# Optimization experiments

Hardware: AMD Instinct MI355X
Metric: run time of the kernel (lower is better)

The kernel has to match this reference:

```python
import jax, jax.numpy as jnp
import numpy as np

NU, NI, D, NNZ = 80000, 40000, 128, 2000000
EPS = 1e-12


def _spmm(dst, src, vals, x, n):
    # sum_e vals[e] * x[src[e]] scattered to dst[e]; A is [n, x.shape[0]] in COO.
    return jax.ops.segment_sum(vals[:, None] * x[src], dst, num_segments=n)


def setup_inputs() -> dict:
    key = jax.random.key(0)
    ks = jax.random.split(key, 24)
    limit = float(np.sqrt(6.0 / (D + D)))  # xavier_uniform
    inp = {
        'user_embedding': jax.random.normal(ks[0], (NU, D), jnp.float32),
        'item_embedding': jax.random.normal(ks[1], (NI, D), jnp.float32),
        'uu_embed0': jax.random.normal(ks[2], (NU, D), jnp.float32),
        'ii_embed0': jax.random.normal(ks[3], (NI, D), jnp.float32),
        'uu_embed1': jax.random.normal(ks[4], (NU, D), jnp.float32),
        'ii_embed1': jax.random.normal(ks[5], (NI, D), jnp.float32),
        'uu_embed2': jax.random.normal(ks[6], (NU, D), jnp.float32),
        'ii_embed2': jax.random.normal(ks[7], (NI, D), jnp.float32),
        'u_w': jax.random.uniform(ks[8], (D, D), jnp.float32, -limit, limit),
        'i_w': jax.random.uniform(ks[9], (D, D), jnp.float32, -limit, limit),
    }
    for b in range(4):
        inp[f'rows{b}'] = jax.random.randint(ks[10 + 3 * b], (NNZ,), 0, NU, jnp.int32)
        inp[f'cols{b}'] = jax.random.randint(ks[11 + 3 * b], (NNZ,), 0, NI, jnp.int32)
        inp[f'vals{b}'] = jax.random.uniform(ks[12 + 3 * b], (NNZ,), jnp.float32)
    return inp


def reference(user_embedding, item_embedding, uu_embed0, ii_embed0, uu_embed1,
              ii_embed1, uu_embed2, ii_embed2, u_w, i_w,
              rows0, cols0, vals0, rows1, cols1, vals1,
              rows2, cols2, vals2, rows3, cols3, vals3):
    nu, ni = user_embedding.shape[0], item_embedding.shape[0]
    # behavior 0 = click, 1 = fav, 2 = cart, 3 = buy
    u0 = _spmm(rows0, cols0, vals0, ii_embed0, nu)
    i0 = _spmm(cols0, rows0, vals0, uu_embed0, ni)
    u1 = _spmm(rows1, cols1, vals1, ii_embed1, nu)
    i1 = _spmm(cols1, rows1, vals1, uu_embed1, ni)
    u2 = _spmm(rows2, cols2, vals2, ii_embed2, nu)
    i2 = _spmm(cols2, rows2, vals2, uu_embed2, ni)
    u3 = _spmm(rows3, cols3, vals3, item_embedding, nu)
    i3 = _spmm(cols3, rows3, vals3, user_embedding, ni)
    user_embeddings = jnp.stack([u0, u1, u2, u3], axis=0)  # [4, NU, D]
    item_embeddings = jnp.stack([i0, i1, i2, i3], axis=0)  # [4, NI, D]
    user_out = jax.nn.sigmoid(jnp.mean(user_embeddings, axis=0) @ u_w)
    item_out = jax.nn.sigmoid(jnp.mean(item_embeddings, axis=0) @ i_w)
    # F.normalize default: L2 over dim=1 (the node axis of the stacked tensor)
    def l2n(x):
        return x / jnp.maximum(jnp.linalg.norm(x, axis=1, keepdims=True), EPS)
    return (user_out, item_out, l2n(user_embeddings), l2n(item_embeddings),
            u0, i0, u1, i1, u2, i2)
```

## Files before the change

### kernel.cpp

```cpp
#include <hip/hip_runtime.h>

#define NU 80000
#define NI 40000
#define DD 128
#define NNZ_E 2000000
#define EPSN 1e-12f
#define BWROWS 256
#define NBU 313
#define NBI 157
#define NBPAD 320
#define BSTRIDE 336
#define BIN_E 8192
#define S2CAP 16384
#define NREP 4

struct EdgePtrs { const int* rows[4]; const int* cols[4]; const float* vals[4]; };

struct GM4 {
  const int* rp[4];
  const int2* pairs[4];
  const unsigned short* xt[4];
  float* out[4];
  float* dup[4];
  float* meanb;
  float* colsums;
  int cbase;
};

__device__ inline unsigned short f2bf(float f) {
  unsigned int u = __float_as_uint(f);
  u += 0x7FFFu + ((u >> 16) & 1u);
  return (unsigned short)(u >> 16);
}

__global__ __launch_bounds__(256) void conv_k(const float* __restrict__ src,
                                              unsigned short* __restrict__ dst, int n4) {
  int stride = blockDim.x * gridDim.x;
  for (int i = blockIdx.x * blockDim.x + threadIdx.x; i < n4; i += stride) {
    float4 f = ((const float4*)src)[i];
    ushort4 h;
    h.x = f2bf(f.x); h.y = f2bf(f.y); h.z = f2bf(f.z); h.w = f2bf(f.w);
    ((ushort4*)dst)[i] = h;
  }
}

__global__ __launch_bounds__(256) void histB_k(EdgePtrs ep, int* cntA) {
  int b = blockIdx.y;
  const int* __restrict__ rows = ep.rows[b];
  const int* __restrict__ cols = ep.cols[b];
  __shared__ int lh[NBU + NBI];
  for (int i = threadIdx.x; i < NBU + NBI; i += blockDim.x) lh[i] = 0;
  __syncthreads();
  int stride = blockDim.x * gridDim.x;
  for (int e = blockIdx.x * blockDim.x + threadIdx.x; e < NNZ_E; e += stride) {
    atomicAdd(&lh[rows[e] >> 8], 1);
    atomicAdd(&lh[NBU + (cols[e] >> 8)], 1);
  }
  __syncthreads();
  int* cu = cntA + (b * 2 + 0) * NBPAD;
  int* ci = cntA + (b * 2 + 1) * NBPAD;
  for (int i = threadIdx.x; i < NBU + NBI; i += blockDim.x) {
    int v = lh[i];
    if (v) {
      if (i < NBU) atomicAdd(&cu[i], v);
      else atomicAdd(&ci[i - NBU], v);
    }
  }
}

__global__ __launch_bounds__(512) void scanb_k(const int* cntA, int* baseA, int* gcurA) {
  __shared__ int wsums[9];
  int a = blockIdx.x;
  int dir = a & 1;
  int n = dir ? NBI : NBU;
  const int* cnt = cntA + a * NBPAD;
  int* base = baseA + a * BSTRIDE;
  int* gcur = gcurA + a * NBPAD;
  int t = threadIdx.x, lane = t & 63, w = t >> 6;
  int v = (t < n) ? cnt[t] : 0;
  int s = v;
  #pragma unroll
  for (int off = 1; off < 64; off <<= 1) {
    int x = __shfl_up(s, off);
    if (lane >= off) s += x;
  }
  if (lane == 63) wsums[w] = s;
  __syncthreads();
  if (t == 0) {
    int run = 0;
    for (int k = 0; k < 8; k++) { int x = wsums[k]; wsums[k] = run; run += x; }
    wsums[8] = run;
  }
  __syncthreads();
  int ex = wsums[w] + s - v;
  if (t < n) { base[t] = ex; gcur[t] = ex; }
  if (t == 0) base[n] = wsums[8];
}

__global__ __launch_bounds__(512) void bin_k(EdgePtrs ep, int b0, int* gcurA, int2* binned) {
  __shared__ int2 stage[BIN_E];
  __shared__ int lh[NBPAD], lscan[NBPAD], lcur[NBPAD], gpos[NBPAD];
  __shared__ int wsums[9];
  int dir = blockIdx.y, j = blockIdx.z, b = b0 + j;
  int NB = dir ? NBI : NBU;
  const int* __restrict__ dst = dir ? ep.cols[b] : ep.rows[b];
  const int* __restrict__ src = dir ? ep.rows[b] : ep.cols[b];
  const float* __restrict__ vals = ep.vals[b];
  int* gcur = gcurA + (b * 2 + dir) * NBPAD;
  int2* out = binned + ((size_t)j * 2 + dir) * NNZ_E;
  int t = threadIdx.x;
  int e0 = blockIdx.x * BIN_E;
  int nh = min(BIN_E, NNZ_E - e0);
  for (int i = t; i < NBPAD; i += 512) lh[i] = 0;
  __syncthreads();
  for (int i = t; i < nh; i += 512) atomicAdd(&lh[dst[e0 + i] >> 8], 1);
  __syncthreads();
  {
    int lane = t & 63, w = t >> 6;
    int v = (t < NB) ? lh[t] : 0;
    int s = v;
    #pragma unroll
    for (int off = 1; off < 64; off <<= 1) {
      int x = __shfl_up(s, off);
      if (lane >= off) s += x;
    }
    if (lane == 63) wsums[w] = s;
    __syncthreads();
    if (t == 0) {
      int run = 0;
      for (int k = 0; k < 8; k++) { int x = wsums[k]; wsums[k] = run; run += x; }
      wsums[8] = run;
    }
    __syncthreads();
    int ex = wsums[w] + s - v;
    if (t < NB) { lscan[t] = ex; lcur[t] = ex; gpos[t] = atomicAdd(&gcur[t], v); }
  }
  __syncthreads();
  for (int i = t; i < nh; i += 512) {
    int d = dst[e0 + i], s = src[e0 + i];
    int k = d >> 8;
    int pos = atomicAdd(&lcur[k], 1);
    stage[pos] = make_int2(s | ((d & 255) << 17), __float_as_int(vals[e0 + i]));
  }
  __syncthreads();
  int w = t >> 6, lane = t & 63;
  for (int k = w; k < NB; k += 8) {
    int c = lh[k];
    const int2* sp = stage + lscan[k];
    int2* gp = out + gpos[k];
    for (int i = lane; i < c; i += 64) gp[i] = sp[i];
  }
}

__global__ __launch_bounds__(512) void sort3_k(int* rpU, int* rpI, int b0,
                                               const int* baseA, int2* binned) {
  __shared__ int2 stage[S2CAP];
  __shared__ int lh[256];
  __shared__ int excl[257];
  __shared__ int lcur[256];
  __shared__ int wsums[5];
  int gb = blockIdx.x;
  int j = gb / (NBU + NBI);
  int r = gb - j * (NBU + NBI);
  int dir = (r >= NBU) ? 1 : 0;
  int k = dir ? (r - NBU) : r;
  int b = b0 + j;
  int n = dir ? NI : NU;
  int* rp = dir ? (rpI + (size_t)b * (NI + 1)) : (rpU + (size_t)b * (NU + 1));
  const int* base = baseA + (b * 2 + dir) * BSTRIDE;
  int2* bb = binned + ((size_t)j * 2 + dir) * NNZ_E;
  int row0 = k << 8;
  int nrows = min(BWROWS, n - row0);
  int base0 = base[k];
  int tot = base[k + 1] - base0;
  int t = threadIdx.x;
  if (t < 256) lh[t] = 0;
  __syncthreads();
  for (int i = t; i < tot; i += 512) atomicAdd(&lh[(bb[base0 + i].x >> 17) & 255], 1);
  __syncthreads();
  int v = 0, s = 0;
  if (t < 256) {
    int lane = t & 63, w = t >> 6;
    v = lh[t]; s = v;
    #pragma unroll
    for (int off = 1; off < 64; off <<= 1) {
      int x = __shfl_up(s, off);
      if (lane >= off) s += x;
    }
    if (lane == 63) wsums[w] = s;
  }
  __syncthreads();
  if (t == 0) {
    int run = 0;
    for (int q = 0; q < 4; q++) { int x = wsums[q]; wsums[q] = run; run += x; }
    wsums[4] = run;
  }
  __syncthreads();
  if (t < 256) {
    int ex = wsums[t >> 6] + s - v;
    excl[t] = ex; lcur[t] = ex;
  }
  if (t == 0) excl[256] = wsums[4];
  __syncthreads();
  if (t <= nrows) rp[row0 + t] = base0 + excl[t];
  for (int i = t; i < tot; i += 512) {
    int2 p = bb[base0 + i];
    int ld = (p.x >> 17) & 255;
    int pos = atomicAdd(&lcur[ld], 1);
    stage[pos] = make_int2(p.x & 0x1FFFF, p.y);
  }
  __syncthreads();
  for (int i = t; i < tot; i += 512) bb[base0 + i] = stage[i];
}

__global__ __launch_bounds__(256) void gather4_k(GM4 gm, int nrows, int ngroups) {
  int gid = blockIdx.x * 8 + (threadIdx.x >> 5);
  int lane = threadIdx.x & 31;
  int t = threadIdx.x;
  float4 sq0 = make_float4(0.f,0.f,0.f,0.f), sq1 = sq0, sq2 = sq0, sq3 = sq0;
  for (int r = gid; r < nrows; r += ngroups) {
    float4 mean = make_float4(0.f,0.f,0.f,0.f);
    #pragma unroll
    for (int b = 0; b < 4; b++) {
      const int* rp = gm.rp[b];
      const int2* __restrict__ pairs = gm.pairs[b];
      const ushort4* __restrict__ x4 = (const ushort4*)gm.xt[b];
      int beg = rp[r], end = rp[r + 1];
      float4 a0 = make_float4(0.f,0.f,0.f,0.f);
      float4 a1 = make_float4(0.f,0.f,0.f,0.f);
      int e = beg;
      for (; e + 3 < end; e += 4) {
        int2 p0 = pairs[e], p1 = pairs[e + 1], p2 = pairs[e + 2], p3 = pairs[e + 3];
        ushort4 h0 = x4[(size_t)p0.x * 32 + lane];
        ushort4 h1 = x4[(size_t)p1.x * 32 + lane];
        ushort4 h2 = x4[(size_t)p2.x * 32 + lane];
        ushort4 h3 = x4[(size_t)p3.x * 32 + lane];
        float v0 = __int_as_float(p0.y), v1 = __int_as_float(p1.y);
        float v2 = __int_as_float(p2.y), v3 = __int_as_float(p3.y);
        a0.x += v0 * __uint_as_float((unsigned)h0.x << 16);
        a0.y += v0 * __uint_as_float((unsigned)h0.y << 16);
        a0.z += v0 * __uint_as_float((unsigned)h0.z << 16);
        a0.w += v0 * __uint_as_float((unsigned)h0.w << 16);
        a1.x += v1 * __uint_as_float((unsigned)h1.x << 16);
        a1.y += v1 * __uint_as_float((unsigned)h1.y << 16);
        a1.z += v1 * __uint_as_float((unsigned)h1.z << 16);
        a1.w += v1 * __uint_as_float((unsigned)h1.w << 16);
        a0.x += v2 * __uint_as_float((unsigned)h2.x << 16);
        a0.y += v2 * __uint_as_float((unsigned)h2.y << 16);
        a0.z += v2 * __uint_as_float((unsigned)h2.z << 16);
        a0.w += v2 * __uint_as_float((unsigned)h2.w << 16);
        a1.x += v3 * __uint_as_float((unsigned)h3.x << 16);
        a1.y += v3 * __uint_as_float((unsigned)h3.y << 16);
        a1.z += v3 * __uint_as_float((unsigned)h3.z << 16);
        a1.w += v3 * __uint_as_float((unsigned)h3.w << 16);
      }
      for (; e < end; e++) {
        int2 p = pairs[e];
        ushort4 h = x4[(size_t)p.x * 32 + lane];
        float v = __int_as_float(p.y);
        a0.x += v * __uint_as_float((unsigned)h.x << 16);
        a0.y += v * __uint_as_float((unsigned)h.y << 16);
        a0.z += v * __uint_as_float((unsigned)h.z << 16);
        a0.w += v * __uint_as_float((unsigned)h.w << 16);
      }
      float4 res = make_float4(a0.x + a1.x, a0.y + a1.y, a0.z + a1.z, a0.w + a1.w);
      ((float4*)gm.out[b])[(size_t)r * 32 + lane] = res;
      if (gm.dup[b]) ((float4*)gm.dup[b])[(size_t)r * 32 + lane] = res;
      mean.x += res.x; mean.y += res.y; mean.z += res.z; mean.w += res.w;
      float4* sqp = (b == 0) ? &sq0 : (b == 1) ? &sq1 : (b == 2) ? &sq2 : &sq3;
      sqp->x += res.x * res.x; sqp->y += res.y * res.y;
      sqp->z += res.z * res.z; sqp->w += res.w * res.w;
    }
    mean.x *= 0.25f; mean.y *= 0.25f; mean.z *= 0.25f; mean.w *= 0.25f;
    ((float4*)gm.meanb)[(size_t)r * 32 + lane] = mean;
  }
  __shared__ float csq[512];
  csq[t] = 0.f; csq[t + 256] = 0.f;
  __syncthreads();
  int cb = lane * 4;
  atomicAdd(&csq[0 * 128 + cb + 0], sq0.x); atomicAdd(&csq[0 * 128 + cb + 1], sq0.y);
  atomicAdd(&csq[0 * 128 + cb + 2], sq0.z); atomicAdd(&csq[0 * 128 + cb + 3], sq0.w);
  atomicAdd(&csq[1 * 128 + cb + 0], sq1.x); atomicAdd(&csq[1 * 128 + cb + 1], sq1.y);
  atomicAdd(&csq[1 * 128 + cb + 2], sq1.z); atomicAdd(&csq[1 * 128 + cb + 3], sq1.w);
  atomicAdd(&csq[2 * 128 + cb + 0], sq2.x); atomicAdd(&csq[2 * 128 + cb + 1], sq2.y);
  atomicAdd(&csq[2 * 128 + cb + 2], sq2.z); atomicAdd(&csq[2 * 128 + cb + 3], sq2.w);
  atomicAdd(&csq[3 * 128 + cb + 0], sq3.x); atomicAdd(&csq[3 * 128 + cb + 1], sq3.y);
  atomicAdd(&csq[3 * 128 + cb + 2], sq3.z); atomicAdd(&csq[3 * 128 + cb + 3], sq3.w);
  __syncthreads();
  float* dst = gm.colsums + (blockIdx.x & (NREP - 1)) * 1024 + gm.cbase;
  atomicAdd(&dst[t], csq[t]);
  atomicAdd(&dst[t + 256], csq[t + 256]);
}

__global__ __launch_bounds__(256) void gather_k(const int* __restrict__ rp, const int2* __restrict__ pairs,
                                                const void* __restrict__ xt, int isbf,
                                                float* __restrict__ out1, float* __restrict__ out2,
                                                int nrows) {
  int gid = blockIdx.x * 8 + (threadIdx.x >> 5);
  int lane = threadIdx.x & 31;
  int tot = gridDim.x * 8;
  for (int r = gid; r < nrows; r += tot) {
    int beg = rp[r], end = rp[r + 1];
    float4 a0 = make_float4(0.f, 0.f, 0.f, 0.f);
    int e = beg;
    if (isbf) {
      const ushort4* __restrict__ x4 = (const ushort4*)xt;
      for (; e < end; e++) {
        int2 p = pairs[e];
        ushort4 h = x4[(size_t)p.x * 32 + lane];
        float v = __int_as_float(p.y);
        a0.x += v * __uint_as_float((unsigned)h.x << 16);
        a0.y += v * __uint_as_float((unsigned)h.y << 16);
        a0.z += v * __uint_as_float((unsigned)h.z << 16);
        a0.w += v * __uint_as_float((unsigned)h.w << 16);
      }
    } else {
      const float4* __restrict__ x4 = (const float4*)xt;
      for (; e < end; e++) {
        int2 p = pairs[e];
        float4 xv = x4[(size_t)p.x * 32 + lane];
        float v = __int_as_float(p.y);
        a0.x += v * xv.x; a0.y += v * xv.y; a0.z += v * xv.z; a0.w += v * xv.w;
      }
    }
    ((float4*)out1)[(size_t)r * 32 + lane] = a0;
    if (out2) ((float4*)out2)[(size_t)r * 32 + lane] = a0;
  }
}

__global__ __launch_bounds__(256) void gemm_sig_m(const float* __restrict__ mean,
                                                  const float* __restrict__ W, float* __restrict__ out,
                                                  int n) {
  __shared__ float wl[DD * DD];
  __shared__ float rl[8][DD];
  for (int i = threadIdx.x; i < DD * DD / 4; i += blockDim.x)
    ((float4*)wl)[i] = ((const float4*)W)[i];
  int c = threadIdx.x & 127;
  int g = threadIdx.x >> 7;
  int row0 = blockIdx.x * 64;
  for (int rr = 0; rr < 64; rr += 8) {
    int rbase = row0 + rr;
    __syncthreads();
    for (int i = threadIdx.x; i < 8 * DD; i += blockDim.x) {
      int lr = i >> 7, lc = i & 127;
      int r = rbase + lr;
      rl[lr][lc] = (r < n) ? mean[(size_t)r * DD + lc] : 0.f;
    }
    __syncthreads();
    float acc0 = 0.f, acc1 = 0.f, acc2 = 0.f, acc3 = 0.f;
    #pragma unroll 4
    for (int k = 0; k < DD; k++) {
      float wv = wl[k * DD + c];
      acc0 += rl[g * 4 + 0][k] * wv;
      acc1 += rl[g * 4 + 1][k] * wv;
      acc2 += rl[g * 4 + 2][k] * wv;
      acc3 += rl[g * 4 + 3][k] * wv;
    }
    float accs[4] = {acc0, acc1, acc2, acc3};
    for (int jj = 0; jj < 4; jj++) {
      int r = rbase + g * 4 + jj;
      if (r < n) out[(size_t)r * DD + c] = 1.f / (1.f + __expf(-accs[jj]));
    }
  }
}

__global__ __launch_bounds__(256) void gemm_sig_k(const float* __restrict__ x, size_t sstride,
                                                  const float* __restrict__ W, float* __restrict__ out,
                                                  int n) {
  __shared__ float wl[DD * DD];
  __shared__ float rl[8][DD];
  for (int i = threadIdx.x; i < DD * DD / 4; i += blockDim.x)
    ((float4*)wl)[i] = ((const float4*)W)[i];
  int c = threadIdx.x & 127;
  int g = threadIdx.x >> 7;
  int row0 = blockIdx.x * 64;
  for (int rr = 0; rr < 64; rr += 8) {
    int rbase = row0 + rr;
    __syncthreads();
    for (int i = threadIdx.x; i < 8 * DD; i += blockDim.x) {
      int lr = i >> 7, lc = i & 127;
      int r = rbase + lr;
      float m = 0.f;
      if (r < n) {
        size_t off = (size_t)r * DD + lc;
        m = 0.25f * (x[off] + x[off + sstride] + x[off + 2 * sstride] + x[off + 3 * sstride]);
      }
      rl[lr][lc] = m;
    }
    __syncthreads();
    float acc0 = 0.f, acc1 = 0.f, acc2 = 0.f, acc3 = 0.f;
    #pragma unroll 4
    for (int k = 0; k < DD; k++) {
      float wv = wl[k * DD + c];
      acc0 += rl[g * 4 + 0][k] * wv;
      acc1 += rl[g * 4 + 1][k] * wv;
      acc2 += rl[g * 4 + 2][k] * wv;
      acc3 += rl[g * 4 + 3][k] * wv;
    }
    float accs[4] = {acc0, acc1, acc2, acc3};
    for (int jj = 0; jj < 4; jj++) {
      int r = rbase + g * 4 + jj;
      if (r < n) out[(size_t)r * DD + c] = 1.f / (1.f + __expf(-accs[jj]));
    }
  }
}

__global__ __launch_bounds__(256) void colsq_k(const float* __restrict__ base, size_t sstride, int n,
                                               float* __restrict__ sums) {
  int b = blockIdx.y;
  const float* x = base + (size_t)b * sstride;
  int c = threadIdx.x & 127;
  int rh = threadIdx.x >> 7;
  float acc = 0.f;
  for (int r = blockIdx.x * 2 + rh; r < n; r += gridDim.x * 2) {
    float v = x[(size_t)r * DD + c];
    acc += v * v;
  }
  __shared__ float red[256];
  red[threadIdx.x] = acc;
  __syncthreads();
  if (threadIdx.x < 128) atomicAdd(&sums[b * DD + threadIdx.x], red[threadIdx.x] + red[threadIdx.x + 128]);
}

__global__ void inv_k(const float* __restrict__ sums, float* __restrict__ inv, int n, int nrep) {
  int i = blockIdx.x * blockDim.x + threadIdx.x;
  if (i < n) {
    float s = 0.f;
    for (int r = 0; r < nrep; r++) s += sums[r * 1024 + i];
    inv[i] = 1.f / fmaxf(sqrtf(s), EPSN);
  }
}

__global__ __launch_bounds__(256) void scaleall_k(float* __restrict__ l2nU, float* __restrict__ l2nI,
                                                  const float* __restrict__ invs) {
  int y = blockIdx.y;
  float4* b4;
  size_t slice;
  if (y < 4) { b4 = (float4*)l2nU + (size_t)y * NU * 32; slice = (size_t)NU * 32; }
  else { b4 = (float4*)l2nI + (size_t)(y - 4) * NI * 32; slice = (size_t)NI * 32; }
  const float4* inv4 = (const float4*)invs + (size_t)y * 32;
  size_t stride = (size_t)blockDim.x * gridDim.x;
  for (size_t i = (size_t)blockIdx.x * blockDim.x + threadIdx.x; i < slice; i += stride) {
    float4 s = inv4[i & 31];
    float4 v = b4[i];
    v.x *= s.x; v.y *= s.y; v.z *= s.z; v.w *= s.w;
    b4[i] = v;
  }
}

extern "C" void kernel_launch(void* const* d_in, const int* in_sizes, int n_in,
                              void* d_out, int out_size, void* d_ws, size_t ws_size,
                              hipStream_t stream) {
  const float* user_emb = (const float*)d_in[0];
  const float* item_emb = (const float*)d_in[1];
  const float* uu[4] = {(const float*)d_in[2], (const float*)d_in[4], (const float*)d_in[6], user_emb};
  const float* ii[4] = {(const float*)d_in[3], (const float*)d_in[5], (const float*)d_in[7], item_emb};
  const float* u_w = (const float*)d_in[8];
  const float* i_w = (const float*)d_in[9];
  EdgePtrs ep;
  for (int b = 0; b < 4; b++) {
    ep.rows[b] = (const int*)d_in[10 + 3 * b];
    ep.cols[b] = (const int*)d_in[11 + 3 * b];
    ep.vals[b] = (const float*)d_in[12 + 3 * b];
  }

  float* out = (float*)d_out;
  float* user_out = out;
  float* item_out = out + (size_t)NU * DD;
  float* l2nU = item_out + (size_t)NI * DD;
  float* l2nI = l2nU + (size_t)4 * NU * DD;
  float* u_slot[3];
  float* i_slot[3];
  {
    float* p = l2nI + (size_t)4 * NI * DD;
    for (int b = 0; b < 3; b++) {
      u_slot[b] = p; p += (size_t)NU * DD;
      i_slot[b] = p; p += (size_t)NI * DD;
    }
  }

  const size_t binsl = (size_t)2 * NNZ_E * 8;
  const size_t item_bf_sz = (size_t)4 * NI * DD * 2;
  const size_t user_bf_sz = (size_t)4 * NU * DD * 2;
  const size_t mean_sz = (size_t)(NU + NI) * DD * 4;
  const size_t smalls = 8u << 20;

  int batchB; bool bfI, bfU;
  if (ws_size >= 4 * binsl + item_bf_sz + user_bf_sz + mean_sz + smalls) { batchB = 4; bfI = bfU = true; }
  else if (ws_size >= 2 * binsl + item_bf_sz + user_bf_sz + smalls) { batchB = 2; bfI = bfU = true; }
  else if (ws_size >= binsl + item_bf_sz + user_bf_sz + smalls) { batchB = 1; bfI = bfU = true; }
  else if (ws_size >= binsl + item_bf_sz + smalls) { batchB = 1; bfI = true; bfU = false; }
  else { batchB = 1; bfI = bfU = false; }

  char* w = (char*)d_ws;
  auto alloc = [&](size_t bytes) {
    char* r = w;
    w += (bytes + 255) & ~(size_t)255;
    return r;
  };
  int2* binned = (int2*)alloc((size_t)batchB * binsl);
  unsigned short* itemB = bfI ? (unsigned short*)alloc(item_bf_sz) : nullptr;
  unsigned short* userB = bfU ? (unsigned short*)alloc(user_bf_sz) : nullptr;
  float* meanU = nullptr;
  float* meanI = nullptr;
  if (batchB == 4) {
    meanU = (float*)alloc((size_t)NU * DD * 4);
    meanI = (float*)alloc((size_t)NI * DD * 4);
  }
  int* cntA = (int*)alloc(4 * 2 * NBPAD * 4);
  int* baseA = (int*)alloc(4 * 2 * BSTRIDE * 4);
  int* gcurA = (int*)alloc(4 * 2 * NBPAD * 4);
  int* rpU = (int*)alloc((size_t)4 * (NU + 1) * 4);
  int* rpI = (int*)alloc((size_t)4 * (NI + 1) * 4);
  float* colsums = (float*)alloc(NREP * 1024 * 4);
  float* invs = (float*)alloc(8 * DD * 4);

  hipMemsetAsync(cntA, 0, 4 * 2 * NBPAD * 4, stream);
  histB_k<<<dim3(256, 4), 256, 0, stream>>>(ep, cntA);
  scanb_k<<<8, 512, 0, stream>>>(cntA, baseA, gcurA);

  const int nchunks = (NNZ_E + BIN_E - 1) / BIN_E;

  if (batchB == 4) {
    bin_k<<<dim3(nchunks, 2, 4), 512, 0, stream>>>(ep, 0, gcurA, binned);
    sort3_k<<<4 * (NBU + NBI), 512, 0, stream>>>(rpU, rpI, 0, baseA, binned);
    for (int b = 0; b < 4; b++)
      conv_k<<<512, 256, 0, stream>>>(ii[b], itemB + (size_t)b * NI * DD, NI * DD / 4);
    for (int b = 0; b < 4; b++)
      conv_k<<<512, 256, 0, stream>>>(uu[b], userB + (size_t)b * NU * DD, NU * DD / 4);
    hipMemsetAsync(colsums, 0, NREP * 1024 * 4, stream);

    GM4 gmU, gmI;
    for (int b = 0; b < 4; b++) {
      gmU.rp[b] = rpU + (size_t)b * (NU + 1);
      gmU.pairs[b] = binned + ((size_t)b * 2 + 0) * NNZ_E;
      gmU.xt[b] = itemB + (size_t)b * NI * DD;
      gmU.out[b] = l2nU + (size_t)b * NU * DD;
      gmU.dup[b] = (b < 3) ? u_slot[b] : nullptr;
      gmI.rp[b] = rpI + (size_t)b * (NI + 1);
      gmI.pairs[b] = binned + ((size_t)b * 2 + 1) * NNZ_E;
      gmI.xt[b] = userB + (size_t)b * NU * DD;
      gmI.out[b] = l2nI + (size_t)b * NI * DD;
      gmI.dup[b] = (b < 3) ? i_slot[b] : nullptr;
    }
    gmU.meanb = meanU; gmU.colsums = colsums; gmU.cbase = 0;
    gmI.meanb = meanI; gmI.colsums = colsums; gmI.cbase = 4 * DD;
    gather4_k<<<2500, 256, 0, stream>>>(gmU, NU, 2500 * 8);
    gather4_k<<<1250, 256, 0, stream>>>(gmI, NI, 1250 * 8);

    inv_k<<<4, 256, 0, stream>>>(colsums, invs, 8 * DD, NREP);
    gemm_sig_m<<<NU / 64, 256, 0, stream>>>(meanU, u_w, user_out, NU);
    gemm_sig_m<<<NI / 64, 256, 0, stream>>>(meanI, i_w, item_out, NI);
    scaleall_k<<<dim3(1024, 8), 256, 0, stream>>>(l2nU, l2nI, invs);
  } else {
    if (bfI)
      for (int b = 0; b < 4; b++)
        conv_k<<<512, 256, 0, stream>>>(ii[b], itemB + (size_t)b * NI * DD, NI * DD / 4);
    if (bfU)
      for (int b = 0; b < 4; b++)
        conv_k<<<512, 256, 0, stream>>>(uu[b], userB + (size_t)b * NU * DD, NU * DD / 4);
    for (int b0 = 0; b0 < 4; b0 += batchB) {
      bin_k<<<dim3(nchunks, 2, batchB), 512, 0, stream>>>(ep, b0, gcurA, binned);
      sort3_k<<<batchB * (NBU + NBI), 512, 0, stream>>>(rpU, rpI, b0, baseA, binned);
      for (int j = 0; j < batchB; j++) {
        int b = b0 + j;
        const void* xt0 = bfI ? (const void*)(itemB + (size_t)b * NI * DD) : (const void*)ii[b];
        const void* xt1 = bfU ? (const void*)(userB + (size_t)b * NU * DD) : (const void*)uu[b];
        gather_k<<<10000, 256, 0, stream>>>(rpU + (size_t)b * (NU + 1),
                                            binned + ((size_t)j * 2 + 0) * NNZ_E, xt0, bfI ? 1 : 0,
                                            l2nU + (size_t)b * NU * DD, (b < 3) ? u_slot[b] : nullptr, NU);
        gather_k<<<5000, 256, 0, stream>>>(rpI + (size_t)b * (NI + 1),
                                           binned + ((size_t)j * 2 + 1) * NNZ_E, xt1, bfU ? 1 : 0,
                                           l2nI + (size_t)b * NI * DD, (b < 3) ? i_slot[b] : nullptr, NI);
      }
    }
    gemm_sig_k<<<NU / 64, 256, 0, stream>>>(l2nU, (size_t)NU * DD, u_w, user_out, NU);
    gemm_sig_k<<<NI / 64, 256, 0, stream>>>(l2nI, (size_t)NI * DD, i_w, item_out, NI);
    hipMemsetAsync(colsums, 0, NREP * 1024 * 4, stream);
    colsq_k<<<dim3(512, 4), 256, 0, stream>>>(l2nU, (size_t)NU * DD, NU, colsums);
    colsq_k<<<dim3(512, 4), 256, 0, stream>>>(l2nI, (size_t)NI * DD, NI, colsums + 4 * DD);
    inv_k<<<4, 256, 0, stream>>>(colsums, invs, 8 * DD, 1);
    scaleall_k<<<dim3(1024, 8), 256, 0, stream>>>(l2nU, l2nI, invs);
  }
}
```

Measured before the change: 1.417 ms.

## Merge conversion, gather, GEMM and scale launches into fewer fused kernels

Replaces the eight per-behavior bf16 conversion launches with one 2D-grid launch. Merges the user and item gather kernels into one grid with direction chosen per block, each warp handling four fixed rows and loading behavior pointers once. Merges the two sigmoid GEMMs into one launch and folds the inverse-norm computation into the scaling kernel. This cuts launch count and lets user and item work share the GPU at once, at the cost of hardcoded grid sizes that assume NU and NI divide evenly into four-row warp groups.

```diff
diff --git a/kernel.cpp b/kernel.cpp
--- a/kernel.cpp
+++ b/kernel.cpp
@@ -13,24 +13,44 @@
 #define BIN_E 8192
 #define S2CAP 16384
 #define NREP 4
+#define GF_NBU 2500
+#define GF_NBI 1250
 
 struct EdgePtrs { const int* rows[4]; const int* cols[4]; const float* vals[4]; };
 
-struct GM4 {
-  const int* rp[4];
-  const int2* pairs[4];
-  const unsigned short* xt[4];
-  float* out[4];
-  float* dup[4];
-  float* meanb;
+struct GAll {
+  const int* rp[2][4];
+  const int2* pairs[2][4];
+  const unsigned short* xt[2][4];
+  float* out[2][4];
+  float* dup[2][4];
+  float* meanb[2];
   float* colsums;
-  int cbase;
 };
+
+struct ConvPtrs { const float* src[8]; unsigned short* dst[8]; int n4[8]; };
 
 __device__ inline unsigned short f2bf(float f) {
   unsigned int u = __float_as_uint(f);
   u += 0x7FFFu + ((u >> 16) & 1u);
   return (unsigned short)(u >> 16);
+}
+__device__ inline float bf2f(unsigned short h) {
+  return __uint_as_float((unsigned)h << 16);
+}
+
+__global__ __launch_bounds__(256) void convA_k(ConvPtrs cp) {
+  int y = blockIdx.y;
+  const float4* __restrict__ src = (const float4*)cp.src[y];
+  ushort4* __restrict__ dst = (ushort4*)cp.dst[y];
+  int n4 = cp.n4[y];
+  int stride = blockDim.x * gridDim.x;
+  for (int i = blockIdx.x * blockDim.x + threadIdx.x; i < n4; i += stride) {
+    float4 f = src[i];
+    ushort4 h;
+    h.x = f2bf(f.x); h.y = f2bf(f.y); h.z = f2bf(f.z); h.w = f2bf(f.w);
+    dst[i] = h;
+  }
 }
 
 __global__ __launch_bounds__(256) void conv_k(const float* __restrict__ src,
@@ -213,21 +233,31 @@
   for (int i = t; i < tot; i += 512) bb[base0 + i] = stage[i];
 }
 
-__global__ __launch_bounds__(256) void gather4_k(GM4 gm, int nrows, int ngroups) {
-  int gid = blockIdx.x * 8 + (threadIdx.x >> 5);
+__global__ __launch_bounds__(256) void gatherF_k(GAll g) {
+  int blk = blockIdx.x;
+  int dir = (blk >= GF_NBU) ? 1 : 0;
+  int lblk = dir ? (blk - GF_NBU) : blk;
+  int gid = lblk * 8 + (threadIdx.x >> 5);
   int lane = threadIdx.x & 31;
   int t = threadIdx.x;
-  float4 sq0 = make_float4(0.f,0.f,0.f,0.f), sq1 = sq0, sq2 = sq0, sq3 = sq0;
-  for (int r = gid; r < nrows; r += ngroups) {
-    float4 mean = make_float4(0.f,0.f,0.f,0.f);
+  int r0 = gid * 4;
+
+  float4 z = make_float4(0.f, 0.f, 0.f, 0.f);
+  float4 mean[4] = {z, z, z, z};
+  float4 sq[4] = {z, z, z, z};
+
+  #pragma unroll
+  for (int b = 0; b < 4; b++) {
+    const int* __restrict__ rp = g.rp[dir][b];
+    const int2* __restrict__ pairs = g.pairs[dir][b];
+    const ushort4* __restrict__ x4 = (const ushort4*)g.xt[dir][b];
+    float4* __restrict__ outp = (float4*)g.out[dir][b];
+    float4* __restrict__ dupp = (float4*)g.dup[dir][b];
     #pragma unroll
-    for (int b = 0; b < 4; b++) {
-      const int* rp = gm.rp[b];
-      const int2* __restrict__ pairs = gm.pairs[b];
-      const ushort4* __restrict__ x4 = (const ushort4*)gm.xt[b];
+    for (int k = 0; k < 4; k++) {
+      int r = r0 + k;
       int beg = rp[r], end = rp[r + 1];
-      float4 a0 = make_float4(0.f,0.f,0.f,0.f);
-      float4 a1 = make_float4(0.f,0.f,0.f,0.f);
+      float4 a0 = z, a1 = z;
       int e = beg;
       for (; e + 3 < end; e += 4) {
         int2 p0 = pairs[e], p1 = pairs[e + 1], p2 = pairs[e + 2], p3 = pairs[e + 3];
@@ -237,57 +267,50 @@
         ushort4 h3 = x4[(size_t)p3.x * 32 + lane];
         float v0 = __int_as_float(p0.y), v1 = __int_as_float(p1.y);
         float v2 = __int_as_float(p2.y), v3 = __int_as_float(p3.y);
-        a0.x += v0 * __uint_as_float((unsigned)h0.x << 16);
-        a0.y += v0 * __uint_as_float((unsigned)h0.y << 16);
-        a0.z += v0 * __uint_as_float((unsigned)h0.z << 16);
-        a0.w += v0 * __uint_as_float((unsigned)h0.w << 16);
-        a1.x += v1 * __uint_as_float((unsigned)h1.x << 16);
-        a1.y += v1 * __uint_as_float((unsigned)h1.y << 16);
-        a1.z += v1 * __uint_as_float((unsigned)h1.z << 16);
-        a1.w += v1 * __uint_as_float((unsigned)h1.w << 16);
-        a0.x += v2 * __uint_as_float((unsigned)h2.x << 16);
-        a0.y += v2 * __uint_as_float((unsigned)h2.y << 16);
-        a0.z += v2 * __uint_as_float((unsigned)h2.z << 16);
-        a0.w += v2 * __uint_as_float((unsigned)h2.w << 16);
-        a1.x += v3 * __uint_as_float((unsigned)h3.x << 16);
-        a1.y += v3 * __uint_as_float((unsigned)h3.y << 16);
-        a1.z += v3 * __uint_as_float((unsigned)h3.z << 16);
-        a1.w += v3 * __uint_as_float((unsigned)h3.w << 16);
+        a0.x += v0 * bf2f(h0.x); a0.y += v0 * bf2f(h0.y);
+        a0.z += v0 * bf2f(h0.z); a0.w += v0 * bf2f(h0.w);
+        a1.x += v1 * bf2f(h1.x); a1.y += v1 * bf2f(h1.y);
+        a1.z += v1 * bf2f(h1.z); a1.w += v1 * bf2f(h1.w);
+        a0.x += v2 * bf2f(h2.x); a0.y += v2 * bf2f(h2.y);
+        a0.z += v2 * bf2f(h2.z); a0.w += v2 * bf2f(h2.w);
+        a1.x += v3 * bf2f(h3.x); a1.y += v3 * bf2f(h3.y);
+        a1.z += v3 * bf2f(h3.z); a1.w += v3 * bf2f(h3.w);
       }
       for (; e < end; e++) {
         int2 p = pairs[e];
         ushort4 h = x4[(size_t)p.x * 32 + lane];
         float v = __int_as_float(p.y);
-        a0.x += v * __uint_as_float((unsigned)h.x << 16);
-        a0.y += v * __uint_as_float((unsigned)h.y << 16);
-        a0.z += v * __uint_as_float((unsigned)h.z << 16);
-        a0.w += v * __uint_as_float((unsigned)h.w << 16);
+        a0.x += v * bf2f(h.x); a0.y += v * bf2f(h.y);
+        a0.z += v * bf2f(h.z); a0.w += v * bf2f(h.w);
       }
       float4 res = make_float4(a0.x + a1.x, a0.y + a1.y, a0.z + a1.z, a0.w + a1.w);
-      ((float4*)gm.out[b])[(size_t)r * 32 + lane] = res;
-      if (gm.dup[b]) ((float4*)gm.dup[b])[(size_t)r * 32 + lane] = res;
-      mean.x += res.x; mean.y += res.y; mean.z += res.z; mean.w += res.w;
-      float4* sqp = (b == 0) ? &sq0 : (b == 1) ? &sq1 : (b == 2) ? &sq2 : &sq3;
-      sqp->x += res.x * res.x; sqp->y += res.y * res.y;
-      sqp->z += res.z * res.z; sqp->w += res.w * res.w;
-    }
-    mean.x *= 0.25f; mean.y *= 0.25f; mean.z *= 0.25f; mean.w *= 0.25f;
-    ((float4*)gm.meanb)[(size_t)r * 32 + lane] = mean;
+      outp[(size_t)r * 32 + lane] = res;
+      if (dupp) dupp[(size_t)r * 32 + lane] = res;
+      mean[k].x += res.x; mean[k].y += res.y; mean[k].z += res.z; mean[k].w += res.w;
+      sq[b].x += res.x * res.x; sq[b].y += res.y * res.y;
+      sq[b].z += res.z * res.z; sq[b].w += res.w * res.w;
+    }
+  }
+  float4* mb = (float4*)g.meanb[dir];
+  #pragma unroll
+  for (int k = 0; k < 4; k++) {
+    float4 m = mean[k];
+    m.x *= 0.25f; m.y *= 0.25f; m.z *= 0.25f; m.w *= 0.25f;
+    mb[(size_t)(r0 + k) * 32 + lane] = m;
   }
   __shared__ float csq[512];
   csq[t] = 0.f; csq[t + 256] = 0.f;
   __syncthreads();
   int cb = lane * 4;
-  atomicAdd(&csq[0 * 128 + cb + 0], sq0.x); atomicAdd(&csq[0 * 128 + cb + 1], sq0.y);
-  atomicAdd(&csq[0 * 128 + cb + 2], sq0.z); atomicAdd(&csq[0 * 128 + cb + 3], sq0.w);
-  atomicAdd(&csq[1 * 128 + cb + 0], sq1.x); atomicAdd(&csq[1 * 128 + cb + 1], sq1.y);
-  atomicAdd(&csq[1 * 128 + cb + 2], sq1.z); atomicAdd(&csq[1 * 128 + cb + 3], sq1.w);
-  atomicAdd(&csq[2 * 128 + cb + 0], sq2.x); atomicAdd(&csq[2 * 128 + cb + 1], sq2.y);
-  atomicAdd(&csq[2 * 128 + cb + 2], sq2.z); atomicAdd(&csq[2 * 128 + cb + 3], sq2.w);
-  atomicAdd(&csq[3 * 128 + cb + 0], sq3.x); atomicAdd(&csq[3 * 128 + cb + 1], sq3.y);
-  atomicAdd(&csq[3 * 128 + cb + 2], sq3.z); atomicAdd(&csq[3 * 128 + cb + 3], sq3.w);
-  __syncthreads();
-  float* dst = gm.colsums + (blockIdx.x & (NREP - 1)) * 1024 + gm.cbase;
+  #pragma unroll
+  for (int b = 0; b < 4; b++) {
+    atomicAdd(&csq[b * 128 + cb + 0], sq[b].x);
+    atomicAdd(&csq[b * 128 + cb + 1], sq[b].y);
+    atomicAdd(&csq[b * 128 + cb + 2], sq[b].z);
+    atomicAdd(&csq[b * 128 + cb + 3], sq[b].w);
+  }
+  __syncthreads();
+  float* dst = g.colsums + (blockIdx.x & (NREP - 1)) * 1024 + dir * 512;
   atomicAdd(&dst[t], csq[t]);
   atomicAdd(&dst[t + 256], csq[t + 256]);
 }
@@ -309,10 +332,8 @@
         int2 p = pairs[e];
         ushort4 h = x4[(size_t)p.x * 32 + lane];
         float v = __int_as_float(p.y);
-        a0.x += v * __uint_as_float((unsigned)h.x << 16);
-        a0.y += v * __uint_as_float((unsigned)h.y << 16);
-        a0.z += v * __uint_as_float((unsigned)h.z << 16);
-        a0.w += v * __uint_as_float((unsigned)h.w << 16);
+        a0.x += v * bf2f(h.x); a0.y += v * bf2f(h.y);
+        a0.z += v * bf2f(h.z); a0.w += v * bf2f(h.w);
       }
     } else {
       const float4* __restrict__ x4 = (const float4*)xt;
@@ -328,16 +349,22 @@
   }
 }
 
-__global__ __launch_bounds__(256) void gemm_sig_m(const float* __restrict__ mean,
-                                                  const float* __restrict__ W, float* __restrict__ out,
-                                                  int n) {
+__global__ __launch_bounds__(256) void gemm2_k(const float* __restrict__ meanU,
+                                               const float* __restrict__ meanI,
+                                               const float* __restrict__ u_w,
+                                               const float* __restrict__ i_w,
+                                               float* __restrict__ user_out,
+                                               float* __restrict__ item_out) {
   __shared__ float wl[DD * DD];
   __shared__ float rl[8][DD];
+  int blk = blockIdx.x;
+  const float* mean; const float* W; float* outp; int n; int row0;
+  if (blk < NU / 64) { mean = meanU; W = u_w; outp = user_out; n = NU; row0 = blk * 64; }
+  else { mean = meanI; W = i_w; outp = item_out; n = NI; row0 = (blk - NU / 64) * 64; }
   for (int i = threadIdx.x; i < DD * DD / 4; i += blockDim.x)
     ((float4*)wl)[i] = ((const float4*)W)[i];
   int c = threadIdx.x & 127;
   int g = threadIdx.x >> 7;
-  int row0 = blockIdx.x * 64;
   for (int rr = 0; rr < 64; rr += 8) {
     int rbase = row0 + rr;
     __syncthreads();
@@ -359,7 +386,7 @@
     float accs[4] = {acc0, acc1, acc2, acc3};
     for (int jj = 0; jj < 4; jj++) {
       int r = rbase + g * 4 + jj;
-      if (r < n) out[(size_t)r * DD + c] = 1.f / (1.f + __expf(-accs[jj]));
+      if (r < n) outp[(size_t)r * DD + c] = 1.f / (1.f + __expf(-accs[jj]));
     }
   }
 }
@@ -431,6 +458,32 @@
   }
 }
 
+__global__ __launch_bounds__(256) void scaleall2_k(float* __restrict__ l2nU, float* __restrict__ l2nI,
+                                                   const float* __restrict__ colsums) {
+  __shared__ float sinv[DD];
+  int y = blockIdx.y;
+  int t = threadIdx.x;
+  if (t < DD) {
+    float s = 0.f;
+    #pragma unroll
+    for (int rr = 0; rr < NREP; rr++) s += colsums[rr * 1024 + y * DD + t];
+    sinv[t] = 1.f / fmaxf(sqrtf(s), EPSN);
+  }
+  __syncthreads();
+  float4* b4;
+  size_t slice;
+  if (y < 4) { b4 = (float4*)l2nU + (size_t)y * NU * 32; slice = (size_t)NU * 32; }
+  else { b4 = (float4*)l2nI + (size_t)(y - 4) * NI * 32; slice = (size_t)NI * 32; }
+  const float4* inv4 = (const float4*)sinv;
+  size_t stride = (size_t)blockDim.x * gridDim.x;
+  for (size_t i = (size_t)blockIdx.x * blockDim.x + threadIdx.x; i < slice; i += stride) {
+    float4 s = inv4[i & 31];
+    float4 v = b4[i];
+    v.x *= s.x; v.y *= s.y; v.z *= s.z; v.w *= s.w;
+    b4[i] = v;
+  }
+}
+
 __global__ __launch_bounds__(256) void scaleall_k(float* __restrict__ l2nU, float* __restrict__ l2nI,
                                                   const float* __restrict__ invs) {
   int y = blockIdx.y;
@@ -524,34 +577,34 @@
   if (batchB == 4) {
     bin_k<<<dim3(nchunks, 2, 4), 512, 0, stream>>>(ep, 0, gcurA, binned);
     sort3_k<<<4 * (NBU + NBI), 512, 0, stream>>>(rpU, rpI, 0, baseA, binned);
-    for (int b = 0; b < 4; b++)
-      conv_k<<<512, 256, 0, stream>>>(ii[b], itemB + (size_t)b * NI * DD, NI * DD / 4);
-    for (int b = 0; b < 4; b++)
-      conv_k<<<512, 256, 0, stream>>>(uu[b], userB + (size_t)b * NU * DD, NU * DD / 4);
+
+    ConvPtrs cp;
+    for (int b = 0; b < 4; b++) {
+      cp.src[b] = ii[b]; cp.dst[b] = itemB + (size_t)b * NI * DD; cp.n4[b] = NI * DD / 4;
+      cp.src[4 + b] = uu[b]; cp.dst[4 + b] = userB + (size_t)b * NU * DD; cp.n4[4 + b] = NU * DD / 4;
+    }
+    convA_k<<<dim3(512, 8), 256, 0, stream>>>(cp);
     hipMemsetAsync(colsums, 0, NREP * 1024 * 4, stream);
 
-    GM4 gmU, gmI;
+    GAll g;
     for (int b = 0; b < 4; b++) {
-      gmU.rp[b] = rpU + (size_t)b * (NU + 1);
-      gmU.pairs[b] = binned + ((size_t)b * 2 + 0) * NNZ_E;
-      gmU.xt[b] = itemB + (size_t)b * NI * DD;
-      gmU.out[b] = l2nU + (size_t)b * NU * DD;
-      gmU.dup[b] = (b < 3) ? u_slot[b] : nullptr;
-      gmI.rp[b] = rpI + (size_t)b * (NI + 1);
-      gmI.pairs[b] = binned + ((size_t)b * 2 + 1) * NNZ_E;
-      gmI.xt[b] = userB + (size_t)b * NU * DD;
-      gmI.out[b] = l2nI + (size_t)b * NI * DD;
-      gmI.dup[b] = (b < 3) ? i_slot[b] : nullptr;
-    }
-    gmU.meanb = meanU; gmU.colsums = colsums; gmU.cbase = 0;
-    gmI.meanb = meanI; gmI.colsums = colsums; gmI.cbase = 4 * DD;
-    gather4_k<<<2500, 256, 0, stream>>>(gmU, NU, 2500 * 8);
-    gather4_k<<<1250, 256, 0, stream>>>(gmI, NI, 1250 * 8);
-
-    inv_k<<<4, 256, 0, stream>>>(colsums, invs, 8 * DD, NREP);
-    gemm_sig_m<<<NU / 64, 256, 0, stream>>>(meanU, u_w, user_out, NU);
-    gemm_sig_m<<<NI / 64, 256, 0, stream>>>(meanI, i_w, item_out, NI);
-    scaleall_k<<<dim3(1024, 8), 256, 0, stream>>>(l2nU, l2nI, invs);
+      g.rp[0][b] = rpU + (size_t)b * (NU + 1);
+      g.pairs[0][b] = binned + ((size_t)b * 2 + 0) * NNZ_E;
+      g.xt[0][b] = itemB + (size_t)b * NI * DD;
+      g.out[0][b] = l2nU + (size_t)b * NU * DD;
+      g.dup[0][b] = (b < 3) ? u_slot[b] : nullptr;
+      g.rp[1][b] = rpI + (size_t)b * (NI + 1);
+      g.pairs[1][b] = binned + ((size_t)b * 2 + 1) * NNZ_E;
+      g.xt[1][b] = userB + (size_t)b * NU * DD;
+      g.out[1][b] = l2nI + (size_t)b * NI * DD;
+      g.dup[1][b] = (b < 3) ? i_slot[b] : nullptr;
+    }
+    g.meanb[0] = meanU; g.meanb[1] = meanI;
+    g.colsums = colsums;
+    gatherF_k<<<GF_NBU + GF_NBI, 256, 0, stream>>>(g);
+
+    gemm2_k<<<NU / 64 + NI / 64, 256, 0, stream>>>(meanU, meanI, u_w, i_w, user_out, item_out);
+    scaleall2_k<<<dim3(1024, 8), 256, 0, stream>>>(l2nU, l2nI, colsums);
   } else {
     if (bfI)
       for (int b = 0; b < 4; b++)
```

After: 1.422 ms. No clear change (+0.4%).
